# Performance work log

Hardware: AMD Instinct MI355X
Metric: run time of the kernel (lower is better)

Reference implementation:

```python
import jax, jax.numpy as jnp
import numpy as np

N = 4194304  # nodes
B = 16384    # graphs
D = 2        # spatial dim
EPS = 1e-12  # F.normalize eps


def _mlp(x, W1, b1, W2, b2, W3, b3, W4, b4, W5, b5):
    h = jax.nn.relu(x @ W1.T + b1)
    h = jax.nn.relu(h @ W2.T + b2)
    h = jax.nn.relu(h @ W3.T + b3)
    h = jax.nn.relu(h @ W4.T + b4)
    return h @ W5.T + b5  # [N,1]


def setup_inputs() -> dict:
    key = jax.random.key(0)
    ks = jax.random.split(key, 16)
    inp = {
        "t": jax.random.normal(ks[0], (N,), jnp.float32),
        "pos": jax.random.normal(ks[1], (N, D), jnp.float32),
        "poi_t": jax.random.normal(ks[2], (B,), jnp.float32),
        "poi_pos": jax.random.normal(ks[3], (B, D), jnp.float32),
        "batch": jnp.sort(jax.random.randint(ks[4], (N,), 0, B, jnp.int64)),
    }
    dims = [(10, 3), (20, 10), (10, 20), (5, 10), (1, 5)]
    for i, (o, ii) in enumerate(dims):
        s = 1.0 / np.sqrt(ii)
        inp[f"W{i+1}"] = jax.random.uniform(ks[5 + 2 * i], (o, ii), jnp.float32, -s, s)
        inp[f"b{i+1}"] = jax.random.uniform(ks[6 + 2 * i], (o,), jnp.float32, -s, s)
    return inp


def reference(t, pos, poi_t, poi_pos, batch, W1, b1, W2, b2, W3, b3, W4, b4, W5, b5):
    num_seg = poi_t.shape[0]
    diff_t = t - poi_t[batch]                      # [N]
    diff_pos = pos - poi_pos[batch]                # [N,D]
    r2 = jnp.sum(diff_pos ** 2, axis=1)            # [N]
    centroid = jax.ops.segment_sum(pos, batch, num_segments=num_seg)  # [B,D]
    diff_centroid = (centroid - poi_pos)[batch]    # [N,D]
    cosine = jnp.sum(diff_pos * diff_centroid, axis=1) / jnp.sqrt(
        r2 * jnp.sum(diff_centroid ** 2, axis=1))  # [N]
    feats = jnp.stack((diff_t, r2, cosine), axis=1)  # [N,3]
    weights = _mlp(feats, W1, b1, W2, b2, W3, b3, W4, b4, W5, b5)  # [N,1]
    norm = jnp.maximum(jnp.linalg.norm(diff_pos, axis=1, keepdims=True), EPS)
    unit = diff_pos / norm                         # F.normalize(diff_pos, dim=1)
    return jax.ops.segment_sum(weights * unit, batch, num_segments=num_seg)  # [B,D]
```

## Files before the change

### kernel.cpp

```cpp
#include <hip/hip_runtime.h>

#define NNODES 4194304
#define NGRAPH 16384

typedef _Float16 half4 __attribute__((ext_vector_type(4)));
typedef float floatx4 __attribute__((ext_vector_type(4)));
typedef unsigned int uint;

__device__ __forceinline__ uint pk_u32(float lo, float hi) {
  return __builtin_bit_cast(uint, __builtin_amdgcn_cvt_pkrtz(lo, hi));
}

__device__ __forceinline__ half4 relu_cvt(floatx4 d) {
  uint2 u;
  u.x = pk_u32(d[0], d[1]);
  u.y = pk_u32(d[2], d[3]);
  half4 h = __builtin_bit_cast(half4, u);
  return __builtin_elementwise_max(h, half4{0, 0, 0, 0});
}

template <int CTRL>
__device__ __forceinline__ float dpp_add(float x) {
  int y = __builtin_amdgcn_update_dpp(0, __builtin_bit_cast(int, x), CTRL,
                                      0xf, 0xf, true);
  return x + __builtin_bit_cast(float, y);
}
__device__ __forceinline__ float wave_sum(float x) {
  x = dpp_add<0x111>(x);
  x = dpp_add<0x112>(x);
  x = dpp_add<0x114>(x);
  x = dpp_add<0x118>(x);
  x = dpp_add<0x142>(x);
  x = dpp_add<0x143>(x);
  return x;
}

__global__ __launch_bounds__(256) void scan_kernel(
    const int* __restrict__ batch, int* __restrict__ start) {
  int i = blockIdx.x * 256 + threadIdx.x;
  int b0 = batch[i];
  if (i == 0) {
    for (int g = 0; g <= b0; ++g) start[g] = 0;
  }
  if (i == NNODES - 1) {
    for (int g = b0 + 1; g <= NGRAPH; ++g) start[g] = NNODES;
  } else {
    int b1 = batch[i + 1];
    for (int g = b0 + 1; g <= b1; ++g) start[g] = i + 1;
  }
}

__global__ void prepack_kernel(
    const float* __restrict__ W1, const float* __restrict__ W2,
    const float* __restrict__ W3, const float* __restrict__ W4,
    const float* __restrict__ W5, const float* __restrict__ B1,
    const float* __restrict__ B2, const float* __restrict__ B3,
    const float* __restrict__ B4, const float* __restrict__ B5,
    uint2* __restrict__ Wf) {
  int p = blockIdx.x * 256 + threadIdx.x;
  if (p >= 448) return;
  int tile = p >> 6, lane = p & 63, row = lane & 15, kb = (lane >> 4) * 4;
  float v[4];
#pragma unroll
  for (int i = 0; i < 4; ++i) {
    int k = kb + i;
    float x = 0.f;
    switch (tile) {
      case 0:
        if (row < 10 && k < 3) x = W1[row * 3 + k];
        if (k == 3) { if (row < 10) x = B1[row]; else if (row == 10) x = 1.f; }
        break;
      case 1:
        if (k < 10) x = W2[row * 10 + k];
        else if (k == 10) x = B2[row];
        break;
      case 2:
        if (row < 4 && k < 10) x = W2[(16 + row) * 10 + k];
        if (k == 10) { if (row < 4) x = B2[16 + row]; else if (row == 4) x = 1.f; }
        break;
      case 3:
        if (row < 10 && k < 16) x = W3[row * 20 + k];
        break;
      case 4:
        if (row < 10 && k < 4) x = W3[row * 20 + 16 + k];
        if (k == 4) { if (row < 10) x = B3[row]; else if (row == 10) x = 1.f; }
        break;
      case 5:
        if (row < 5 && k < 10) x = W4[row * 10 + k];
        if (k == 10) { if (row < 5) x = B4[row]; else if (row == 5) x = 1.f; }
        break;
      default:
        if (row == 0 && k < 5) x = W5[k];
        if (row == 0 && k == 5) x = B5[0];
        break;
    }
    v[i] = x;
  }
  Wf[p] = uint2{pk_u32(v[0], v[1]), pk_u32(v[2], v[3])};
}

__device__ __forceinline__ floatx4 mfma16(half4 a, half4 b, floatx4 c) {
  return __builtin_amdgcn_mfma_f32_16x16x16f16(a, b, c, 0, 0, 0);
}

__global__ __launch_bounds__(256, 8) void fused_kernel(
    const float* __restrict__ t, const float2* __restrict__ pos,
    const float* __restrict__ poi_t, const float2* __restrict__ poi_pos,
    const int* __restrict__ start, const uint2* __restrict__ Wf,
    float* __restrict__ out) {
  const int tid = threadIdx.x;
  const int lane = tid & 63;
  const int wid = tid >> 6;
  const int col = lane & 15;
  const int koct = lane >> 4;
  const int g = blockIdx.x * 4 + wid;

  int s = start[g], e = start[g + 1];
  float2 pp = poi_pos[g];
  float pt = poi_t[g];
  int niter = (e - s + 63) >> 6;

  float cx = 0.f, cy = 0.f;
  for (int it = 0; it < niter; ++it) {
    int idx = s + it * 64 + lane;
    bool valid = idx < e;
    int idxc = min(idx, NNODES - 1);
    float2 p = pos[idxc];
    if (valid) { cx += p.x; cy += p.y; }
  }
  cx = wave_sum(cx);
  cy = wave_sum(cy);
  cx = __shfl(cx, 63);
  cy = __shfl(cy, 63);
  float dcx = cx - pp.x, dcy = cy - pp.y;
  float invc = rsqrtf(dcx * dcx + dcy * dcy);
  float ucx = dcx * invc, ucy = dcy * invc;

  half4 wa[7];
#pragma unroll
  for (int k = 0; k < 7; ++k)
    wa[k] = __builtin_bit_cast(half4, Wf[k * 64 + lane]);
  floatx4 cz{0.f, 0.f, 0.f, 0.f};

  float ox = 0.f, oy = 0.f;
  for (int it = 0; it < niter; ++it) {
    int idx = s + it * 64 + lane;
    bool valid = idx < e;
    int idxc = min(idx, NNODES - 1);
    float tv = t[idxc];
    float2 p = pos[idxc];
    float f0 = tv - pt;
    float dpx = p.x - pp.x, dpy = p.y - pp.y;
    float f1 = dpx * dpx + dpy * dpy;
    float invr = rsqrtf(f1);
    float f2 = (dpx * ucx + dpy * ucy) * invr;
    int fx = (int)pk_u32(f0, f1);
    int fy = (int)pk_u32(f2, 1.0f);

    half4 b1[4];
#pragma unroll
    for (int g2 = 0; g2 < 4; ++g2) {
      int src = g2 * 16 + col;
      uint2 fr;
      fr.x = (uint)__shfl(fx, src);
      fr.y = (uint)__shfl(fy, src);
      b1[g2] = __builtin_bit_cast(half4, fr);
    }

    floatx4 d[4];
    half4 a[4];
#pragma unroll
    for (int c = 0; c < 4; ++c) d[c] = mfma16(wa[0], b1[c], cz);
#pragma unroll
    for (int c = 0; c < 4; ++c) a[c] = relu_cvt(d[c]);

    floatx4 d2[4];
    half4 a3a[4], a3b[4];
#pragma unroll
    for (int c = 0; c < 4; ++c) d2[c] = mfma16(wa[1], a[c], cz);
#pragma unroll
    for (int c = 0; c < 4; ++c) a3a[c] = relu_cvt(d2[c]);
#pragma unroll
    for (int c = 0; c < 4; ++c) d2[c] = mfma16(wa[2], a[c], cz);
#pragma unroll
    for (int c = 0; c < 4; ++c) a3b[c] = relu_cvt(d2[c]);

#pragma unroll
    for (int c = 0; c < 4; ++c) d[c] = mfma16(wa[3], a3a[c], cz);
#pragma unroll
    for (int c = 0; c < 4; ++c) d[c] = mfma16(wa[4], a3b[c], d[c]);
#pragma unroll
    for (int c = 0; c < 4; ++c) a[c] = relu_cvt(d[c]);

#pragma unroll
    for (int c = 0; c < 4; ++c) d[c] = mfma16(wa[5], a[c], cz);
#pragma unroll
    for (int c = 0; c < 4; ++c) a[c] = relu_cvt(d[c]);

#pragma unroll
    for (int c = 0; c < 4; ++c) d[c] = mfma16(wa[6], a[c], cz);

    float wg0 = __shfl(d[0][0], col);
    float wg1 = __shfl(d[1][0], col);
    float wg2 = __shfl(d[2][0], col);
    float wg3 = __shfl(d[3][0], col);
    float w = wg0;
    w = (koct == 1) ? wg1 : w;
    w = (koct == 2) ? wg2 : w;
    w = (koct == 3) ? wg3 : w;
    float invn = (f1 > 0.f) ? invr : 0.f;
    if (valid) {
      ox += w * dpx * invn;
      oy += w * dpy * invn;
    }
  }

  ox = wave_sum(ox);
  oy = wave_sum(oy);
  if (lane == 63) ((float2*)out)[g] = float2{ox, oy};
}

extern "C" void kernel_launch(void* const* d_in, const int* in_sizes, int n_in,
                              void* d_out, int out_size, void* d_ws,
                              size_t ws_size, hipStream_t stream) {
  const float* t = (const float*)d_in[0];
  const float2* pos = (const float2*)d_in[1];
  const float* poi_t = (const float*)d_in[2];
  const float2* poi_pos = (const float2*)d_in[3];
  const int* batch = (const int*)d_in[4];
  const float* W1 = (const float*)d_in[5];
  const float* B1 = (const float*)d_in[6];
  const float* W2 = (const float*)d_in[7];
  const float* B2 = (const float*)d_in[8];
  const float* W3 = (const float*)d_in[9];
  const float* B3 = (const float*)d_in[10];
  const float* W4 = (const float*)d_in[11];
  const float* B4 = (const float*)d_in[12];
  const float* W5 = (const float*)d_in[13];
  const float* B5 = (const float*)d_in[14];
  float* out = (float*)d_out;

  int* start = (int*)d_ws;
  uint2* Wf = (uint2*)(start + NGRAPH + 1);

  prepack_kernel<<<2, 256, 0, stream>>>(W1, W2, W3, W4, W5, B1, B2, B3, B4,
                                        B5, Wf);
  scan_kernel<<<NNODES / 256, 256, 0, stream>>>(batch, start);
  fused_kernel<<<NGRAPH / 4, 256, 0, stream>>>(t, pos, poi_t, poi_pos, start,
                                               Wf, out);
}
```

Baseline: 46.66 us.

## Software-prefetch next node tile and enlarge blocks to 16 waves

Both per-graph loops now load the next 64-node chunk of t/pos before working on the current one. This double-buffering is meant to hide global memory latency behind the MFMA chain. The block size also grows from 256 to 1024 threads, 16 graphs per block. That cuts the block count, but the launch-bounds change may push up register pressure and lower occupancy.

```diff
diff --git a/kernel.cpp b/kernel.cpp
--- a/kernel.cpp
+++ b/kernel.cpp
@@ -103,7 +103,7 @@
   return __builtin_amdgcn_mfma_f32_16x16x16f16(a, b, c, 0, 0, 0);
 }
 
-__global__ __launch_bounds__(256, 8) void fused_kernel(
+__global__ __launch_bounds__(1024, 8) void fused_kernel(
     const float* __restrict__ t, const float2* __restrict__ pos,
     const float* __restrict__ poi_t, const float2* __restrict__ poi_pos,
     const int* __restrict__ start, const uint2* __restrict__ Wf,
@@ -113,7 +113,7 @@
   const int wid = tid >> 6;
   const int col = lane & 15;
   const int koct = lane >> 4;
-  const int g = blockIdx.x * 4 + wid;
+  const int g = blockIdx.x * 16 + wid;
 
   int s = start[g], e = start[g + 1];
   float2 pp = poi_pos[g];
@@ -121,12 +121,17 @@
   int niter = (e - s + 63) >> 6;
 
   float cx = 0.f, cy = 0.f;
-  for (int it = 0; it < niter; ++it) {
-    int idx = s + it * 64 + lane;
-    bool valid = idx < e;
-    int idxc = min(idx, NNODES - 1);
-    float2 p = pos[idxc];
-    if (valid) { cx += p.x; cy += p.y; }
+  {
+    int idx0 = s + lane;
+    float2 pA = pos[min(idx0, NNODES - 1)];
+    for (int it = 0; it < niter; ++it) {
+      int nidx = s + (it + 1) * 64 + lane;
+      float2 pB;
+      if (it + 1 < niter) pB = pos[min(nidx, NNODES - 1)];
+      int idx = s + it * 64 + lane;
+      if (idx < e) { cx += pA.x; cy += pA.y; }
+      pA = pB;
+    }
   }
   cx = wave_sum(cx);
   cy = wave_sum(cy);
@@ -143,75 +148,88 @@
   floatx4 cz{0.f, 0.f, 0.f, 0.f};
 
   float ox = 0.f, oy = 0.f;
-  for (int it = 0; it < niter; ++it) {
-    int idx = s + it * 64 + lane;
-    bool valid = idx < e;
-    int idxc = min(idx, NNODES - 1);
-    float tv = t[idxc];
-    float2 p = pos[idxc];
-    float f0 = tv - pt;
-    float dpx = p.x - pp.x, dpy = p.y - pp.y;
-    float f1 = dpx * dpx + dpy * dpy;
-    float invr = rsqrtf(f1);
-    float f2 = (dpx * ucx + dpy * ucy) * invr;
-    int fx = (int)pk_u32(f0, f1);
-    int fy = (int)pk_u32(f2, 1.0f);
-
-    half4 b1[4];
-#pragma unroll
-    for (int g2 = 0; g2 < 4; ++g2) {
-      int src = g2 * 16 + col;
-      uint2 fr;
-      fr.x = (uint)__shfl(fx, src);
-      fr.y = (uint)__shfl(fy, src);
-      b1[g2] = __builtin_bit_cast(half4, fr);
-    }
-
-    floatx4 d[4];
-    half4 a[4];
-#pragma unroll
-    for (int c = 0; c < 4; ++c) d[c] = mfma16(wa[0], b1[c], cz);
-#pragma unroll
-    for (int c = 0; c < 4; ++c) a[c] = relu_cvt(d[c]);
-
-    floatx4 d2[4];
-    half4 a3a[4], a3b[4];
-#pragma unroll
-    for (int c = 0; c < 4; ++c) d2[c] = mfma16(wa[1], a[c], cz);
-#pragma unroll
-    for (int c = 0; c < 4; ++c) a3a[c] = relu_cvt(d2[c]);
-#pragma unroll
-    for (int c = 0; c < 4; ++c) d2[c] = mfma16(wa[2], a[c], cz);
-#pragma unroll
-    for (int c = 0; c < 4; ++c) a3b[c] = relu_cvt(d2[c]);
-
-#pragma unroll
-    for (int c = 0; c < 4; ++c) d[c] = mfma16(wa[3], a3a[c], cz);
-#pragma unroll
-    for (int c = 0; c < 4; ++c) d[c] = mfma16(wa[4], a3b[c], d[c]);
-#pragma unroll
-    for (int c = 0; c < 4; ++c) a[c] = relu_cvt(d[c]);
-
-#pragma unroll
-    for (int c = 0; c < 4; ++c) d[c] = mfma16(wa[5], a[c], cz);
-#pragma unroll
-    for (int c = 0; c < 4; ++c) a[c] = relu_cvt(d[c]);
-
-#pragma unroll
-    for (int c = 0; c < 4; ++c) d[c] = mfma16(wa[6], a[c], cz);
-
-    float wg0 = __shfl(d[0][0], col);
-    float wg1 = __shfl(d[1][0], col);
-    float wg2 = __shfl(d[2][0], col);
-    float wg3 = __shfl(d[3][0], col);
-    float w = wg0;
-    w = (koct == 1) ? wg1 : w;
-    w = (koct == 2) ? wg2 : w;
-    w = (koct == 3) ? wg3 : w;
-    float invn = (f1 > 0.f) ? invr : 0.f;
-    if (valid) {
-      ox += w * dpx * invn;
-      oy += w * dpy * invn;
+  {
+    int idx0c = min(s + lane, NNODES - 1);
+    float tvA = t[idx0c];
+    float2 pvA = pos[idx0c];
+    for (int it = 0; it < niter; ++it) {
+      float tvB;
+      float2 pvB;
+      if (it + 1 < niter) {
+        int nidxc = min(s + (it + 1) * 64 + lane, NNODES - 1);
+        tvB = t[nidxc];
+        pvB = pos[nidxc];
+      }
+
+      int idx = s + it * 64 + lane;
+      bool valid = idx < e;
+      float f0 = tvA - pt;
+      float dpx = pvA.x - pp.x, dpy = pvA.y - pp.y;
+      float f1 = dpx * dpx + dpy * dpy;
+      float invr = rsqrtf(f1);
+      float f2 = (dpx * ucx + dpy * ucy) * invr;
+      int fx = (int)pk_u32(f0, f1);
+      int fy = (int)pk_u32(f2, 1.0f);
+
+      half4 b1[4];
+#pragma unroll
+      for (int g2 = 0; g2 < 4; ++g2) {
+        int src = g2 * 16 + col;
+        uint2 fr;
+        fr.x = (uint)__shfl(fx, src);
+        fr.y = (uint)__shfl(fy, src);
+        b1[g2] = __builtin_bit_cast(half4, fr);
+      }
+
+      floatx4 d[4];
+      half4 a[4];
+#pragma unroll
+      for (int c = 0; c < 4; ++c) d[c] = mfma16(wa[0], b1[c], cz);
+#pragma unroll
+      for (int c = 0; c < 4; ++c) a[c] = relu_cvt(d[c]);
+
+      floatx4 d2[4];
+      half4 a3a[4], a3b[4];
+#pragma unroll
+      for (int c = 0; c < 4; ++c) d2[c] = mfma16(wa[1], a[c], cz);
+#pragma unroll
+      for (int c = 0; c < 4; ++c) a3a[c] = relu_cvt(d2[c]);
+#pragma unroll
+      for (int c = 0; c < 4; ++c) d2[c] = mfma16(wa[2], a[c], cz);
+#pragma unroll
+      for (int c = 0; c < 4; ++c) a3b[c] = relu_cvt(d2[c]);
+
+#pragma unroll
+      for (int c = 0; c < 4; ++c) d[c] = mfma16(wa[3], a3a[c], cz);
+#pragma unroll
+      for (int c = 0; c < 4; ++c) d[c] = mfma16(wa[4], a3b[c], d[c]);
+#pragma unroll
+      for (int c = 0; c < 4; ++c) a[c] = relu_cvt(d[c]);
+
+#pragma unroll
+      for (int c = 0; c < 4; ++c) d[c] = mfma16(wa[5], a[c], cz);
+#pragma unroll
+      for (int c = 0; c < 4; ++c) a[c] = relu_cvt(d[c]);
+
+#pragma unroll
+      for (int c = 0; c < 4; ++c) d[c] = mfma16(wa[6], a[c], cz);
+
+      float wg0 = __shfl(d[0][0], col);
+      float wg1 = __shfl(d[1][0], col);
+      float wg2 = __shfl(d[2][0], col);
+      float wg3 = __shfl(d[3][0], col);
+      float w = wg0;
+      w = (koct == 1) ? wg1 : w;
+      w = (koct == 2) ? wg2 : w;
+      w = (koct == 3) ? wg3 : w;
+      float invn = (f1 > 0.f) ? invr : 0.f;
+      if (valid) {
+        ox += w * dpx * invn;
+        oy += w * dpy * invn;
+      }
+
+      tvA = tvB;
+      pvA = pvB;
     }
   }
 
@@ -246,6 +264,6 @@
   prepack_kernel<<<2, 256, 0, stream>>>(W1, W2, W3, W4, W5, B1, B2, B3, B4,
                                         B5, Wf);
   scan_kernel<<<NNODES / 256, 256, 0, stream>>>(batch, start);
-  fused_kernel<<<NGRAPH / 4, 256, 0, stream>>>(t, pos, poi_t, poi_pos, start,
-                                               Wf, out);
-}
+  fused_kernel<<<NGRAPH / 16, 1024, 0, stream>>>(t, pos, poi_t, poi_pos,
+                                                 start, Wf, out);
+}
```

Result: no change. 46.28 us (median of 2 runs) (-0.8%).
